# Kernel optimization log

Hardware: AMD Instinct MI355X
Metric: run time of the kernel (lower is better)

Reference implementation:

```python
import jax, jax.numpy as jnp
import numpy as np

TEMPERATURE = 8.0  # sqrt(d_head=64)
MASK_FILL = -1e9


def setup_inputs() -> dict:
    key = jax.random.key(0)
    kq, kk, kv, km = jax.random.split(key, 4)
    B, H, L, D = 4, 16, 2048, 64
    return {
        "query": jax.random.normal(kq, (B, H, L, D), dtype=jnp.float32),
        "key": jax.random.normal(kk, (B, H, L, D), dtype=jnp.float32),
        "value": jax.random.normal(kv, (B, H, L, D), dtype=jnp.float32),
        "mask": jax.random.randint(km, (B, 1, L, L), 0, 2, dtype=jnp.int32),
    }


def reference(query, key, value, mask):
    # scores: [B, H, Lq, Lk]
    scores = jnp.einsum("bhqd,bhkd->bhqk", query / TEMPERATURE, key)
    scores = jnp.where(mask == 0, MASK_FILL, scores)
    # sigmoid attention (no row normalization); dropout omitted (eval mode)
    attn = jax.nn.sigmoid(scores)
    output = jnp.einsum("bhqk,bhkd->bhqd", attn, value)
    return (output, attn)
```

## Files before the change

kernel.cpp:

```cpp
#include <hip/hip_runtime.h>
#include <hip/hip_bf16.h>
#include <stdint.h>

#define B_ 4
#define H_ 16
#define L_ 2048
#define D_ 64
#define BH (B_ * H_)

typedef __attribute__((ext_vector_type(8))) short short8;
typedef __attribute__((ext_vector_type(4))) float f32x4;

__device__ __forceinline__ short b16(float f) {
  __hip_bfloat16 h = __float2bfloat16(f);
  return __builtin_bit_cast(short, h);
}

__global__ __launch_bounds__(256) void vt_kernel(const float* __restrict__ V,
                                                 unsigned short* __restrict__ Vt) {
  __shared__ unsigned short lds[64 * 68];
  int bid = blockIdx.x;
  int bh  = bid >> 5;
  int kt  = bid & 31;
  int t   = threadIdx.x;
  const float* vsrc = V + ((size_t)bh * L_ + (size_t)kt * 64) * D_;
#pragma unroll
  for (int i = 0; i < 4; ++i) {
    int f4  = i * 256 + t;
    int row = f4 >> 4;
    int c4  = (f4 & 15) << 2;
    float4 v = *reinterpret_cast<const float4*>(vsrc + row * D_ + c4);
    ushort4 u;
    u.x = (unsigned short)b16(v.x);
    u.y = (unsigned short)b16(v.y);
    u.z = (unsigned short)b16(v.z);
    u.w = (unsigned short)b16(v.w);
    *reinterpret_cast<ushort4*>(&lds[row * 68 + c4]) = u;
  }
  __syncthreads();
  unsigned short* dst = Vt + (size_t)bh * D_ * L_ + (size_t)kt * 64;
#pragma unroll
  for (int i = 0; i < 8; ++i) {
    int c  = i * 256 + t;
    int d  = c >> 5;
    int k2 = (c & 31) * 2;
    unsigned int lo = lds[(k2 + 0) * 68 + d];
    unsigned int hi = lds[(k2 + 1) * 68 + d];
    *reinterpret_cast<unsigned int*>(dst + d * L_ + k2) = lo | (hi << 16);
  }
}

__global__ __launch_bounds__(256) void attn_kernel(
    const float* __restrict__ Q, const float* __restrict__ K,
    const int* __restrict__ M, const unsigned short* __restrict__ Vt,
    float* __restrict__ O, float* __restrict__ A) {
  __shared__ unsigned short Kl[64 * 64];
  __shared__ unsigned short Vl[64 * 64];
  __shared__ unsigned short Pl[64 * 64];

  int wg  = blockIdx.x;
  int swz = (wg & 7) * 256 + (wg >> 3);
  int bh  = swz >> 5;
  int qt  = swz & 31;

  int t    = threadIdx.x;
  int lane = t & 63;
  int w    = t >> 6;
  int wr   = w >> 1;
  int wc   = w & 1;
  int lr   = lane & 15;
  int lg   = lane >> 4;

  short8 qf[2][2];
  const float* qbase = Q + ((size_t)bh * L_ + (size_t)qt * 64 + wr * 32) * D_;
#pragma unroll
  for (int m = 0; m < 2; ++m) {
#pragma unroll
    for (int ks = 0; ks < 2; ++ks) {
      const float4* p = reinterpret_cast<const float4*>(qbase + (m * 16 + lr) * D_ + ks * 32 + lg * 8);
      float4 a = p[0], b = p[1];
      qf[m][ks] = (short8){b16(a.x), b16(a.y), b16(a.z), b16(a.w),
                           b16(b.x), b16(b.y), b16(b.z), b16(b.w)};
    }
  }

  f32x4 o[2][2] = {};
  const int* mbase = M + (size_t)(bh >> 4) * L_ * L_;
  float* abase = A + (size_t)bh * L_ * L_;
  const float* kbase0 = K + (size_t)bh * L_ * D_;
  const unsigned short* vbase0 = Vt + (size_t)bh * D_ * L_;
  int qrow = qt * 64 + wr * 32;

  for (int ki = 0; ki < 32; ++ki) {
    int k0 = ki * 64;

    int mv[2][2][4];
#pragma unroll
    for (int m = 0; m < 2; ++m)
#pragma unroll
      for (int n = 0; n < 2; ++n)
#pragma unroll
        for (int r = 0; r < 4; ++r)
          mv[m][n][r] = mbase[(size_t)(qrow + m * 16 + lg * 4 + r) * L_ + k0 + wc * 32 + n * 16 + lr];

    __syncthreads();

    const float* ksrc = kbase0 + (size_t)k0 * D_;
#pragma unroll
    for (int i = 0; i < 4; ++i) {
      int f4  = i * 256 + t;
      int row = f4 >> 4;
      int c4  = (f4 & 15) << 2;
      float4 v = *reinterpret_cast<const float4*>(ksrc + row * D_ + c4);
      ushort4 u;
      u.x = (unsigned short)b16(v.x);
      u.y = (unsigned short)b16(v.y);
      u.z = (unsigned short)b16(v.z);
      u.w = (unsigned short)b16(v.w);
      *reinterpret_cast<ushort4*>(&Kl[row * 64 + (c4 ^ ((row & 7) << 3))]) = u;
    }
    const unsigned short* vsrc = vbase0 + k0;
#pragma unroll
    for (int i = 0; i < 2; ++i) {
      int g   = i * 256 + t;
      int row = g >> 3;
      int c0  = (g & 7) << 3;
      uint4 v = *reinterpret_cast<const uint4*>(vsrc + (size_t)row * L_ + c0);
      *reinterpret_cast<uint4*>(&Vl[row * 64 + (c0 ^ ((row & 7) << 3))]) = v;
    }
    __syncthreads();

    f32x4 s[2][2] = {};
#pragma unroll
    for (int ks = 0; ks < 2; ++ks) {
      short8 kf[2];
#pragma unroll
      for (int n = 0; n < 2; ++n) {
        int row = wc * 32 + n * 16 + lr;
        int col = ks * 32 + lg * 8;
        kf[n] = *reinterpret_cast<const short8*>(&Kl[row * 64 + (col ^ ((row & 7) << 3))]);
      }
#pragma unroll
      for (int m = 0; m < 2; ++m)
#pragma unroll
        for (int n = 0; n < 2; ++n)
          s[m][n] = __builtin_amdgcn_mfma_f32_16x16x32_bf16(qf[m][ks], kf[n], s[m][n], 0, 0, 0);
    }

#pragma unroll
    for (int m = 0; m < 2; ++m) {
#pragma unroll
      for (int n = 0; n < 2; ++n) {
        int kcol = k0 + wc * 32 + n * 16 + lr;
        int pq0  = wr * 32 + m * 16 + lg * 4;
        int pk   = wc * 32 + n * 16 + lr;
#pragma unroll
        for (int r = 0; r < 4; ++r) {
          float sc = s[m][n][r] * 0.125f;
          float at = 0.0f;
          if (mv[m][n][r] != 0)
            at = __builtin_amdgcn_rcpf(1.0f + __expf(-sc));
          __builtin_nontemporal_store(at, &abase[(size_t)(qrow + m * 16 + lg * 4 + r) * L_ + kcol]);
          int pq = pq0 + r;
          Pl[pq * 64 + (pk ^ ((pq & 7) << 3))] = (unsigned short)b16(at);
        }
      }
    }
    __syncthreads();

#pragma unroll
    for (int ks = 0; ks < 2; ++ks) {
      short8 pf[2], vf[2];
#pragma unroll
      for (int m = 0; m < 2; ++m) {
        int row = wr * 32 + m * 16 + lr;
        int col = ks * 32 + lg * 8;
        pf[m] = *reinterpret_cast<const short8*>(&Pl[row * 64 + (col ^ ((row & 7) << 3))]);
      }
#pragma unroll
      for (int n = 0; n < 2; ++n) {
        int row = wc * 32 + n * 16 + lr;
        int col = ks * 32 + lg * 8;
        vf[n] = *reinterpret_cast<const short8*>(&Vl[row * 64 + (col ^ ((row & 7) << 3))]);
      }
#pragma unroll
      for (int m = 0; m < 2; ++m)
#pragma unroll
        for (int n = 0; n < 2; ++n)
          o[m][n] = __builtin_amdgcn_mfma_f32_16x16x32_bf16(pf[m], vf[n], o[m][n], 0, 0, 0);
    }
  }

  float* obase = O + ((size_t)bh * L_ + (size_t)qt * 64 + wr * 32) * D_;
#pragma unroll
  for (int m = 0; m < 2; ++m)
#pragma unroll
    for (int n = 0; n < 2; ++n)
#pragma unroll
      for (int r = 0; r < 4; ++r)
        __builtin_nontemporal_store(o[m][n][r],
            &obase[(m * 16 + lg * 4 + r) * D_ + wc * 32 + n * 16 + lr]);
}

extern "C" void kernel_launch(void* const* d_in, const int* in_sizes, int n_in,
                              void* d_out, int out_size, void* d_ws, size_t ws_size,
                              hipStream_t stream) {
  (void)in_sizes; (void)n_in; (void)out_size; (void)ws_size;
  const float* Q = (const float*)d_in[0];
  const float* K = (const float*)d_in[1];
  const float* V = (const float*)d_in[2];
  const int*   M = (const int*)d_in[3];
  float* O = (float*)d_out;
  float* A = (float*)d_out + (size_t)BH * L_ * D_;
  unsigned short* Vt = (unsigned short*)d_ws;

  vt_kernel<<<BH * (L_ / 64), 256, 0, stream>>>(V, Vt);
  attn_kernel<<<BH * (L_ / 64), 256, 0, stream>>>(Q, K, M, Vt, O, A);
}
```

Baseline: 353.3 us.

## Pre-tile K/V in bf16, double-buffer via direct LDS loads, vectorize attn stores

Adds preprocessing kernels that write K and transposed V as pre-swizzled bf16 tiles into workspace. The attention kernel then double-buffers these tiles into LDS with global_load_lds, overlapping loads with compute. It also swaps the MFMA operand order so each lane holds four consecutive key columns, which allows 16-byte mask loads and 16-byte nontemporal stores of the attention matrix. The new path needs more workspace and falls back to the old kernels otherwise.

```diff
diff --git a/kernel.cpp b/kernel.cpp
--- a/kernel.cpp
+++ b/kernel.cpp
@@ -14,6 +14,214 @@
 __device__ __forceinline__ short b16(float f) {
   __hip_bfloat16 h = __float2bfloat16(f);
   return __builtin_bit_cast(short, h);
+}
+
+typedef __attribute__((address_space(1))) const unsigned int guint_t;
+typedef __attribute__((address_space(3))) unsigned int luint_t;
+
+__device__ __forceinline__ void glds16(const void* g, void* l) {
+  __builtin_amdgcn_global_load_lds((guint_t*)g, (luint_t*)l, 16, 0, 0);
+}
+
+__device__ __forceinline__ void stage_tile(const unsigned short* __restrict__ src,
+                                           unsigned short* dst, int t) {
+  int w = t >> 6, lane = t & 63;
+  glds16(src + w * 1024 + lane * 8,       dst + w * 1024);
+  glds16(src + w * 1024 + 512 + lane * 8, dst + w * 1024 + 512);
+}
+
+__global__ __launch_bounds__(256) void kb_kernel(const float* __restrict__ K,
+                                                 unsigned short* __restrict__ Kb) {
+  int bid = blockIdx.x;
+  int t   = threadIdx.x;
+  const float* src = K + (size_t)bid * 64 * D_;
+  unsigned short* dst = Kb + (size_t)bid * 4096;
+#pragma unroll
+  for (int i = 0; i < 4; ++i) {
+    int f4  = i * 256 + t;
+    int row = f4 >> 4;
+    int c4  = (f4 & 15) << 2;
+    float4 v = *reinterpret_cast<const float4*>(src + row * D_ + c4);
+    ushort4 u;
+    u.x = (unsigned short)b16(v.x);
+    u.y = (unsigned short)b16(v.y);
+    u.z = (unsigned short)b16(v.z);
+    u.w = (unsigned short)b16(v.w);
+    *reinterpret_cast<ushort4*>(&dst[row * 64 + (c4 ^ ((row & 7) << 3))]) = u;
+  }
+}
+
+__global__ __launch_bounds__(256) void vtb_kernel(const float* __restrict__ V,
+                                                  unsigned short* __restrict__ Vb) {
+  __shared__ unsigned short lds[64 * 68];
+  int bid = blockIdx.x;
+  int t   = threadIdx.x;
+  const float* src = V + (size_t)bid * 64 * D_;
+#pragma unroll
+  for (int i = 0; i < 4; ++i) {
+    int f4  = i * 256 + t;
+    int row = f4 >> 4;
+    int c4  = (f4 & 15) << 2;
+    float4 v = *reinterpret_cast<const float4*>(src + row * D_ + c4);
+    ushort4 u;
+    u.x = (unsigned short)b16(v.x);
+    u.y = (unsigned short)b16(v.y);
+    u.z = (unsigned short)b16(v.z);
+    u.w = (unsigned short)b16(v.w);
+    *reinterpret_cast<ushort4*>(&lds[row * 68 + c4]) = u;
+  }
+  __syncthreads();
+  unsigned short* dst = Vb + (size_t)bid * 4096;
+#pragma unroll
+  for (int i = 0; i < 4; ++i) {
+    int g  = i * 256 + t;
+    int r  = g >> 4;
+    int c4 = (g & 15) << 2;
+    ushort4 u;
+    u.x = lds[(c4 + 0) * 68 + r];
+    u.y = lds[(c4 + 1) * 68 + r];
+    u.z = lds[(c4 + 2) * 68 + r];
+    u.w = lds[(c4 + 3) * 68 + r];
+    *reinterpret_cast<ushort4*>(&dst[r * 64 + (c4 ^ ((r & 7) << 3))]) = u;
+  }
+}
+
+__global__ __launch_bounds__(256) void attn2_kernel(
+    const float* __restrict__ Q, const int* __restrict__ M,
+    const unsigned short* __restrict__ Kb, const unsigned short* __restrict__ Vb,
+    float* __restrict__ O, float* __restrict__ A) {
+  __shared__ __align__(16) unsigned short Kl[2][4096];
+  __shared__ __align__(16) unsigned short Vl[2][4096];
+  __shared__ __align__(16) unsigned short Pl[4096];
+
+  int wg  = blockIdx.x;
+  int swz = (wg & 7) * 256 + (wg >> 3);
+  int bh  = swz >> 5;
+  int qt  = swz & 31;
+
+  int t    = threadIdx.x;
+  int lane = t & 63;
+  int w    = t >> 6;
+  int wr   = w >> 1;
+  int wc   = w & 1;
+  int lr   = lane & 15;
+  int lg   = lane >> 4;
+
+  short8 qf[2][2];
+  const float* qbase = Q + ((size_t)bh * L_ + (size_t)qt * 64 + wr * 32) * D_;
+#pragma unroll
+  for (int m = 0; m < 2; ++m) {
+#pragma unroll
+    for (int ks = 0; ks < 2; ++ks) {
+      const float4* p = reinterpret_cast<const float4*>(qbase + (m * 16 + lr) * D_ + ks * 32 + lg * 8);
+      float4 a = p[0], b = p[1];
+      qf[m][ks] = (short8){b16(a.x), b16(a.y), b16(a.z), b16(a.w),
+                           b16(b.x), b16(b.y), b16(b.z), b16(b.w)};
+    }
+  }
+
+  f32x4 o[2][2] = {};
+  const int* mbase = M + (size_t)(bh >> 4) * L_ * L_;
+  float* abase = A + (size_t)bh * L_ * L_;
+  const unsigned short* kb = Kb + (size_t)bh * 32 * 4096;
+  const unsigned short* vb = Vb + (size_t)bh * 32 * 4096;
+  int qrow = qt * 64 + wr * 32;
+
+  stage_tile(kb, Kl[0], t);
+  stage_tile(vb, Vl[0], t);
+  __syncthreads();
+
+  for (int ki = 0; ki < 32; ++ki) {
+    int cur = ki & 1;
+    int k0  = ki * 64;
+
+    if (ki + 1 < 32) {
+      stage_tile(kb + (size_t)(ki + 1) * 4096, Kl[cur ^ 1], t);
+      stage_tile(vb + (size_t)(ki + 1) * 4096, Vl[cur ^ 1], t);
+    }
+
+    int4 mv[2][2];
+#pragma unroll
+    for (int m = 0; m < 2; ++m)
+#pragma unroll
+      for (int n = 0; n < 2; ++n)
+        mv[m][n] = *reinterpret_cast<const int4*>(
+            mbase + (size_t)(qrow + m * 16 + lr) * L_ + k0 + wc * 32 + n * 16 + lg * 4);
+
+    f32x4 s[2][2] = {};
+#pragma unroll
+    for (int ks = 0; ks < 2; ++ks) {
+      short8 kf[2];
+#pragma unroll
+      for (int n = 0; n < 2; ++n) {
+        int row = wc * 32 + n * 16 + lr;
+        int col = ks * 32 + lg * 8;
+        kf[n] = *reinterpret_cast<const short8*>(&Kl[cur][row * 64 + (col ^ ((row & 7) << 3))]);
+      }
+#pragma unroll
+      for (int m = 0; m < 2; ++m)
+#pragma unroll
+        for (int n = 0; n < 2; ++n)
+          s[m][n] = __builtin_amdgcn_mfma_f32_16x16x32_bf16(kf[n], qf[m][ks], s[m][n], 0, 0, 0);
+    }
+
+#pragma unroll
+    for (int m = 0; m < 2; ++m) {
+#pragma unroll
+      for (int n = 0; n < 2; ++n) {
+        f32x4 f;
+        ushort4 u;
+#pragma unroll
+        for (int r = 0; r < 4; ++r) {
+          float sc = s[m][n][r] * 0.125f;
+          float at = ((&mv[m][n].x)[r] != 0)
+                         ? __builtin_amdgcn_rcpf(1.0f + __expf(-sc))
+                         : 0.0f;
+          f[r] = at;
+          (&u.x)[r] = (unsigned short)b16(at);
+        }
+        __builtin_nontemporal_store(f, reinterpret_cast<f32x4*>(
+            abase + (size_t)(qrow + m * 16 + lr) * L_ + k0 + wc * 32 + n * 16 + lg * 4));
+        int q  = wr * 32 + m * 16 + lr;
+        int kl = wc * 32 + n * 16 + lg * 4;
+        *reinterpret_cast<ushort4*>(&Pl[q * 64 + (kl ^ ((q & 7) << 3))]) = u;
+      }
+    }
+    __syncthreads();
+
+#pragma unroll
+    for (int ks = 0; ks < 2; ++ks) {
+      short8 pf[2], vf[2];
+#pragma unroll
+      for (int m = 0; m < 2; ++m) {
+        int row = wr * 32 + m * 16 + lr;
+        int col = ks * 32 + lg * 8;
+        pf[m] = *reinterpret_cast<const short8*>(&Pl[row * 64 + (col ^ ((row & 7) << 3))]);
+      }
+#pragma unroll
+      for (int n = 0; n < 2; ++n) {
+        int row = wc * 32 + n * 16 + lr;
+        int col = ks * 32 + lg * 8;
+        vf[n] = *reinterpret_cast<const short8*>(&Vl[cur][row * 64 + (col ^ ((row & 7) << 3))]);
+      }
+#pragma unroll
+      for (int m = 0; m < 2; ++m)
+#pragma unroll
+        for (int n = 0; n < 2; ++n)
+          o[m][n] = __builtin_amdgcn_mfma_f32_16x16x32_bf16(pf[m], vf[n], o[m][n], 0, 0, 0);
+    }
+    __syncthreads();
+  }
+
+  float* obase = O + ((size_t)bh * L_ + (size_t)qt * 64 + wr * 32) * D_;
+#pragma unroll
+  for (int m = 0; m < 2; ++m)
+#pragma unroll
+    for (int n = 0; n < 2; ++n)
+#pragma unroll
+      for (int r = 0; r < 4; ++r)
+        __builtin_nontemporal_store(o[m][n][r],
+            &obase[(m * 16 + lg * 4 + r) * D_ + wc * 32 + n * 16 + lr]);
 }
 
 __global__ __launch_bounds__(256) void vt_kernel(const float* __restrict__ V,
@@ -93,7 +301,6 @@
 
   for (int ki = 0; ki < 32; ++ki) {
     int k0 = ki * 64;
-
     int mv[2][2][4];
 #pragma unroll
     for (int m = 0; m < 2; ++m)
@@ -205,15 +412,24 @@
 extern "C" void kernel_launch(void* const* d_in, const int* in_sizes, int n_in,
                               void* d_out, int out_size, void* d_ws, size_t ws_size,
                               hipStream_t stream) {
-  (void)in_sizes; (void)n_in; (void)out_size; (void)ws_size;
+  (void)in_sizes; (void)n_in; (void)out_size;
   const float* Q = (const float*)d_in[0];
   const float* K = (const float*)d_in[1];
   const float* V = (const float*)d_in[2];
   const int*   M = (const int*)d_in[3];
   float* O = (float*)d_out;
   float* A = (float*)d_out + (size_t)BH * L_ * D_;
-  unsigned short* Vt = (unsigned short*)d_ws;
-
-  vt_kernel<<<BH * (L_ / 64), 256, 0, stream>>>(V, Vt);
-  attn_kernel<<<BH * (L_ / 64), 256, 0, stream>>>(Q, K, M, Vt, O, A);
-}
+
+  const size_t tile_bytes = (size_t)BH * 32 * 4096 * 2;
+  if (ws_size >= 2 * tile_bytes) {
+    unsigned short* Kb = (unsigned short*)d_ws;
+    unsigned short* Vb = (unsigned short*)d_ws + (size_t)BH * 32 * 4096;
+    kb_kernel<<<BH * 32, 256, 0, stream>>>(K, Kb);
+    vtb_kernel<<<BH * 32, 256, 0, stream>>>(V, Vb);
+    attn2_kernel<<<BH * 32, 256, 0, stream>>>(Q, M, Kb, Vb, O, A);
+  } else {
+    unsigned short* Vt = (unsigned short*)d_ws;
+    vt_kernel<<<BH * 32, 256, 0, stream>>>(V, Vt);
+    attn_kernel<<<BH * 32, 256, 0, stream>>>(Q, K, M, Vt, O, A);
+  }
+}
```

Result: slower. 422.3 us (+19.5%).

## Transpose QK MFMA for vectorized attn/mask access and remap blocks for mask reuse

Applied to the files above, without the earlier changes.

Swaps the MFMA operand order so each lane holds four consecutive key columns of one query row. Mask loads become int4 and attention-matrix stores become 128-bit nontemporal stores, replacing scalar strided accesses. The workgroup-to-(b,h,qt) mapping is changed so all heads of a batch sharing the same mask tiles run on the same XCD, improving L2 reuse of the mask. It also folds the 1/8 scale into Q, uses exp2 directly, and sets a launch-bounds occupancy hint, with a small precision change from scaling Q before the bf16 conversion.

```diff
diff --git a/kernel.cpp b/kernel.cpp
--- a/kernel.cpp
+++ b/kernel.cpp
@@ -50,7 +50,7 @@
   }
 }
 
-__global__ __launch_bounds__(256) void attn_kernel(
+__global__ __launch_bounds__(256, 4) void attn3_kernel(
     const float* __restrict__ Q, const float* __restrict__ K,
     const int* __restrict__ M, const unsigned short* __restrict__ Vt,
     float* __restrict__ O, float* __restrict__ A) {
@@ -59,9 +59,13 @@
   __shared__ unsigned short Pl[64 * 64];
 
   int wg  = blockIdx.x;
-  int swz = (wg & 7) * 256 + (wg >> 3);
-  int bh  = swz >> 5;
-  int qt  = swz & 31;
+  int xcd = wg & 7;
+  int j   = wg >> 3;
+  int g   = xcd * 16 + (j & 15);
+  int b   = g >> 5;
+  int qt  = g & 31;
+  int h   = j >> 4;
+  int bh  = b * 16 + h;
 
   int t    = threadIdx.x;
   int lane = t & 63;
@@ -78,14 +82,14 @@
 #pragma unroll
     for (int ks = 0; ks < 2; ++ks) {
       const float4* p = reinterpret_cast<const float4*>(qbase + (m * 16 + lr) * D_ + ks * 32 + lg * 8);
-      float4 a = p[0], b = p[1];
-      qf[m][ks] = (short8){b16(a.x), b16(a.y), b16(a.z), b16(a.w),
-                           b16(b.x), b16(b.y), b16(b.z), b16(b.w)};
+      float4 a = p[0], c = p[1];
+      qf[m][ks] = (short8){b16(a.x * 0.125f), b16(a.y * 0.125f), b16(a.z * 0.125f), b16(a.w * 0.125f),
+                           b16(c.x * 0.125f), b16(c.y * 0.125f), b16(c.z * 0.125f), b16(c.w * 0.125f)};
     }
   }
 
   f32x4 o[2][2] = {};
-  const int* mbase = M + (size_t)(bh >> 4) * L_ * L_;
+  const int* mbase = M + (size_t)b * L_ * L_;
   float* abase = A + (size_t)bh * L_ * L_;
   const float* kbase0 = K + (size_t)bh * L_ * D_;
   const unsigned short* vbase0 = Vt + (size_t)bh * D_ * L_;
@@ -94,14 +98,13 @@
   for (int ki = 0; ki < 32; ++ki) {
     int k0 = ki * 64;
 
-    int mv[2][2][4];
+    int4 mv[2][2];
 #pragma unroll
     for (int m = 0; m < 2; ++m)
 #pragma unroll
       for (int n = 0; n < 2; ++n)
-#pragma unroll
-        for (int r = 0; r < 4; ++r)
-          mv[m][n][r] = mbase[(size_t)(qrow + m * 16 + lg * 4 + r) * L_ + k0 + wc * 32 + n * 16 + lr];
+        mv[m][n] = *reinterpret_cast<const int4*>(
+            mbase + (size_t)(qrow + m * 16 + lr) * L_ + k0 + wc * 32 + n * 16 + lg * 4);
 
     __syncthreads();
 
@@ -122,9 +125,9 @@
     const unsigned short* vsrc = vbase0 + k0;
 #pragma unroll
     for (int i = 0; i < 2; ++i) {
-      int g   = i * 256 + t;
-      int row = g >> 3;
-      int c0  = (g & 7) << 3;
+      int gidx = i * 256 + t;
+      int row  = gidx >> 3;
+      int c0   = (gidx & 7) << 3;
       uint4 v = *reinterpret_cast<const uint4*>(vsrc + (size_t)row * L_ + c0);
       *reinterpret_cast<uint4*>(&Vl[row * 64 + (c0 ^ ((row & 7) << 3))]) = v;
     }
@@ -144,26 +147,30 @@
       for (int m = 0; m < 2; ++m)
 #pragma unroll
         for (int n = 0; n < 2; ++n)
-          s[m][n] = __builtin_amdgcn_mfma_f32_16x16x32_bf16(qf[m][ks], kf[n], s[m][n], 0, 0, 0);
+          s[m][n] = __builtin_amdgcn_mfma_f32_16x16x32_bf16(kf[n], qf[m][ks], s[m][n], 0, 0, 0);
     }
 
 #pragma unroll
     for (int m = 0; m < 2; ++m) {
 #pragma unroll
       for (int n = 0; n < 2; ++n) {
-        int kcol = k0 + wc * 32 + n * 16 + lr;
-        int pq0  = wr * 32 + m * 16 + lg * 4;
-        int pk   = wc * 32 + n * 16 + lr;
+        f32x4 f;
+        ushort4 u;
 #pragma unroll
         for (int r = 0; r < 4; ++r) {
-          float sc = s[m][n][r] * 0.125f;
-          float at = 0.0f;
-          if (mv[m][n][r] != 0)
-            at = __builtin_amdgcn_rcpf(1.0f + __expf(-sc));
-          __builtin_nontemporal_store(at, &abase[(size_t)(qrow + m * 16 + lg * 4 + r) * L_ + kcol]);
-          int pq = pq0 + r;
-          Pl[pq * 64 + (pk ^ ((pq & 7) << 3))] = (unsigned short)b16(at);
+          float sv = s[m][n][r];
+          float e  = __builtin_amdgcn_exp2f(sv * -1.44269504f);
+          float at = ((&mv[m][n].x)[r] != 0)
+                         ? __builtin_amdgcn_rcpf(1.0f + e)
+                         : 0.0f;
+          f[r] = at;
+          (&u.x)[r] = (unsigned short)b16(at);
         }
+        __builtin_nontemporal_store(f, reinterpret_cast<f32x4*>(
+            abase + (size_t)(qrow + m * 16 + lr) * L_ + k0 + wc * 32 + n * 16 + lg * 4));
+        int q  = wr * 32 + m * 16 + lr;
+        int kl = wc * 32 + n * 16 + lg * 4;
+        *reinterpret_cast<ushort4*>(&Pl[q * 64 + (kl ^ ((q & 7) << 3))]) = u;
       }
     }
     __syncthreads();
@@ -214,6 +221,6 @@
   float* A = (float*)d_out + (size_t)BH * L_ * D_;
   unsigned short* Vt = (unsigned short*)d_ws;
 
-  vt_kernel<<<BH * (L_ / 64), 256, 0, stream>>>(V, Vt);
-  attn_kernel<<<BH * (L_ / 64), 256, 0, stream>>>(Q, K, M, Vt, O, A);
-}
+  vt_kernel<<<BH * 32, 256, 0, stream>>>(V, Vt);
+  attn3_kernel<<<BH * 32, 256, 0, stream>>>(Q, K, M, Vt, O, A);
+}
```

After: 319.6 us. -9.6%, faster.
